# Kernel optimization log

Hardware: AMD Instinct MI355X
Metric: run time of the kernel (lower is better)

Reference implementation:

```python
import jax, jax.numpy as jnp
import numpy as np

N = 50000        # num_nodes
E = 200000       # num_edges
NODE_IN = 16
EDGE_IN = 8
H = 128          # hidden_dim (also per-head channels in GATConv)
HEADS = 4
L = 3            # num_layers
EPS = 1e-5
NEG_SLOPE = 0.2  # PyG GATConv default


def layer_norm(x, g, b):
    mu = jnp.mean(x, axis=-1, keepdims=True)
    v = jnp.var(x, axis=-1, keepdims=True)
    return (x - mu) * jax.lax.rsqrt(v + EPS) * g + b


def batch_norm_eval(x, g, b, rm, rv):
    return (x - rm) * jax.lax.rsqrt(rv + EPS) * g + b


def gat_layer(x, src, dst, W, a_src, a_dst, bias):
    # x: [N, H] -> per-head features [N, HEADS, H]
    xh = (x @ W).reshape(N, HEADS, H)
    al_src = jnp.sum(xh * a_src, axis=-1)  # [N, HEADS]
    al_dst = jnp.sum(xh * a_dst, axis=-1)  # [N, HEADS]
    alpha = jax.nn.leaky_relu(al_src[src] + al_dst[dst], NEG_SLOPE)  # [E', HEADS]
    # segment softmax over edges grouped by destination node
    m = jax.ops.segment_max(alpha, dst, num_segments=N)
    e = jnp.exp(alpha - m[dst])
    s = jax.ops.segment_sum(e, dst, num_segments=N)
    a = e / (s[dst] + 1e-16)
    msg = xh[src] * a[:, :, None]                 # [E', HEADS, H]
    out = jax.ops.segment_sum(msg, dst, num_segments=N)  # [N, HEADS, H]
    return jnp.mean(out, axis=1) + bias           # concat=False -> head mean


def setup_inputs() -> dict:
    key = jax.random.key(0)
    ks = jax.random.split(key, 24)
    s = 0.1
    inp = {
        "x": jax.random.normal(ks[0], (N, NODE_IN), jnp.float32),
        "edge_index": jax.random.randint(ks[1], (2, E), 0, N, jnp.int32),
        "edge_attr": jax.random.normal(ks[2], (E, EDGE_IN), jnp.float32),
        "shock_mask_nodes": jax.random.randint(ks[3], (N,), 0, 2, jnp.int32),
        # node encoder
        "enc_w": jax.random.normal(ks[4], (NODE_IN + 2, H), jnp.float32) * s,
        "enc_b": jnp.zeros((H,), jnp.float32),
        "enc_ln_g": jnp.ones((H,), jnp.float32),
        "enc_ln_b": jnp.zeros((H,), jnp.float32),
        # GAT layers (stacked over L)
        "gat_w": jax.random.normal(ks[5], (L, H, HEADS * H), jnp.float32) * s,
        "gat_att_src": jax.random.normal(ks[6], (L, HEADS, H), jnp.float32) * s,
        "gat_att_dst": jax.random.normal(ks[7], (L, HEADS, H), jnp.float32) * s,
        "gat_bias": jnp.zeros((L, H), jnp.float32),
        # BatchNorm (eval mode: running stats)
        "bn_g": jnp.ones((L, H), jnp.float32),
        "bn_b": jnp.zeros((L, H), jnp.float32),
        "bn_mean": jax.random.normal(ks[8], (L, H), jnp.float32) * 0.01,
        "bn_var": jnp.ones((L, H), jnp.float32),
        # edge MLP: (2H + EDGE_IN) -> H -> H//2 -> 1
        "em1_w": jax.random.normal(ks[9], (2 * H + EDGE_IN, H), jnp.float32) * s,
        "em1_b": jnp.zeros((H,), jnp.float32),
        "em_ln_g": jnp.ones((H,), jnp.float32),
        "em_ln_b": jnp.zeros((H,), jnp.float32),
        "em2_w": jax.random.normal(ks[10], (H, H // 2), jnp.float32) * s,
        "em2_b": jnp.zeros((H // 2,), jnp.float32),
        "em3_w": jax.random.normal(ks[11], (H // 2, 1), jnp.float32) * s,
        "em3_b": jnp.zeros((1,), jnp.float32),
    }
    return inp


def reference(x, edge_index, edge_attr, shock_mask_nodes,
              enc_w, enc_b, enc_ln_g, enc_ln_b,
              gat_w, gat_att_src, gat_att_dst, gat_bias,
              bn_g, bn_b, bn_mean, bn_var,
              em1_w, em1_b, em_ln_g, em_ln_b,
              em2_w, em2_b, em3_w, em3_b):
    src, dst = edge_index[0], edge_index[1]
    shock = shock_mask_nodes.astype(jnp.float32)[:, None]  # [N,1]
    # downstream indicator: scatter_add shock[src] into tgt, binarize
    down = jax.ops.segment_sum(shock[src, 0], dst, num_segments=N)
    down = (down > 0).astype(jnp.float32)[:, None]
    xa = jnp.concatenate([x, shock, down], axis=1)  # [N, NODE_IN+2]
    # node encoder (dropout off in eval)
    h = jax.nn.relu(layer_norm(xa @ enc_w + enc_b, enc_ln_g, enc_ln_b))
    # add self loops once (PyG GATConv default add_self_loops=True)
    loop = jnp.arange(N, dtype=src.dtype)
    src_sl = jnp.concatenate([src, loop])
    dst_sl = jnp.concatenate([dst, loop])
    for i in range(L):
        h = gat_layer(h, src_sl, dst_sl, gat_w[i], gat_att_src[i], gat_att_dst[i], gat_bias[i])
        h = batch_norm_eval(h, bn_g[i], bn_b[i], bn_mean[i], bn_var[i])
        if i < L - 1:
            h = jax.nn.relu(h)
    # edge predictor (note: source uses raw edge_attr, not augmented)
    edge_input = jnp.concatenate([h[src], h[dst], edge_attr], axis=1)  # [E, 2H+EDGE_IN]
    z = jax.nn.relu(layer_norm(edge_input @ em1_w + em1_b, em_ln_g, em_ln_b))
    z = jax.nn.relu(z @ em2_w + em2_b)
    delta = (z @ em3_w + em3_b)[:, 0]  # [E]
    return delta
```

## Files before the change

kernel.cpp:

```cpp
#include <hip/hip_runtime.h>
#include <hip/hip_bf16.h>


#define N_NODES 50000
#define N_EDGES 200000
#define ETOT    (N_EDGES + N_NODES)
#define HID     128
#define LN_EPS  1e-5f
#define NEG     0.2f
#define NSB     196

typedef __hip_bfloat16 bf16;
typedef __attribute__((ext_vector_type(8))) short v8s;
typedef __attribute__((ext_vector_type(4))) float v4f;
#define MFMA(a, b, c) __builtin_amdgcn_mfma_f32_16x16x32_bf16(a, b, c, 0, 0, 0)

__device__ __forceinline__ float b2f(unsigned short s) {
    return __uint_as_float(((unsigned int)s) << 16);
}
__device__ __forceinline__ unsigned short f2b(float f) {
    __hip_bfloat16 h = __float2bfloat16(f);
    return *reinterpret_cast<unsigned short*>(&h);
}
__device__ __forceinline__ unsigned int pack2(float a, float b) {
    return (unsigned int)f2b(a) | ((unsigned int)f2b(b) << 16);
}
__device__ __forceinline__ float pread(const void* p, size_t i, int isbf) {
    if (isbf) return b2f(((const unsigned short*)p)[i]);
    return ((const float*)p)[i];
}

__global__ void k_fill(float* out, int n, float v) {
    int i = blockIdx.x * blockDim.x + threadIdx.x;
    if (i < n) out[i] = v;
}

__global__ void k_detect(const unsigned short* __restrict__ xbuf,
                         int* __restrict__ flag) {
    int sane = 0;
    for (int j = threadIdx.x; j < 4096; j += 64) {
        unsigned short v = xbuf[2 * j];
        int e = (v >> 7) & 0xFF;
        if (v == 0 || (e > 96 && e < 160)) sane++;
    }
    for (int off = 32; off > 0; off >>= 1) sane += __shfl_down(sane, off);
    if (threadIdx.x == 0) flag[0] = (sane * 10 >= 4096 * 9) ? 1 : 0;
}

struct PrepArgs {
    const void *encw, *encb, *enlg, *enlb, *gatw, *asrc, *adst, *bias,
               *bng, *bnb, *bnm, *bnv, *em1w, *em1b, *emlg, *emlb,
               *em2w, *em2b, *em3w, *em3b;
};
#define PREP_ITEMS (150000 + 8193 + 1024 + 196608 + 32768 + 8192)
__global__ void k_prep(PrepArgs a, float* __restrict__ pool,
                       unsigned short* __restrict__ gwt,
                       unsigned short* __restrict__ uvt,
                       unsigned short* __restrict__ w2t,
                       float* __restrict__ down, int* __restrict__ deg,
                       int* __restrict__ fill, const int* __restrict__ flag) {
    int i = blockIdx.x * 256 + threadIdx.x;
    int bf = flag[0];
    if (i < 150000) {
        int which = i / 50000, idx = i - which * 50000;
        if (which == 0) down[idx] = 0.f;
        else if (which == 1) deg[idx] = 0;
        else fill[idx] = 0;
        return;
    }
    i -= 150000;
    if (i < 8193) {
        const void* s; int off;
        if      (i < 2304) { s = a.encw; off = 0;    }
        else if (i < 2432) { s = a.encb; off = 2304; }
        else if (i < 2560) { s = a.enlg; off = 2432; }
        else if (i < 2688) { s = a.enlb; off = 2560; }
        else if (i < 4224) { s = a.asrc; off = 2688; }
        else if (i < 5760) { s = a.adst; off = 4224; }
        else if (i < 6144) { s = a.bias; off = 5760; }
        else if (i < 6528) { s = a.bng;  off = 6144; }
        else if (i < 6912) { s = a.bnb;  off = 6528; }
        else if (i < 7296) { s = a.bnm;  off = 6912; }
        else if (i < 7680) { s = a.bnv;  off = 7296; }
        else if (i < 7808) { s = a.em1b; off = 7680; }
        else if (i < 7936) { s = a.emlg; off = 7808; }
        else if (i < 8064) { s = a.emlb; off = 7936; }
        else if (i < 8128) { s = a.em2b; off = 8064; }
        else if (i < 8192) { s = a.em3w; off = 8128; }
        else               { s = a.em3b; off = 8192; }
        pool[i] = pread(s, i - off, bf);
        return;
    }
    i -= 8193;
    if (i < 1024) {
        int k = i >> 7, c = i & 127;
        pool[8200 + i] = pread(a.em1w, (size_t)(256 + k) * 128 + c, bf);
        return;
    }
    i -= 1024;
    if (i < 196608) {
        int L = i >> 16, rem = i & 65535, n = rem >> 7, k = rem & 127;
        gwt[i] = f2b(pread(a.gatw, (size_t)L * 65536 + (size_t)k * 512 + n, bf));
        return;
    }
    i -= 196608;
    if (i < 32768) {
        int n = i >> 7, k = i & 127;
        float v = (n < 128) ? pread(a.em1w, (size_t)k * 128 + n, bf)
                            : pread(a.em1w, (size_t)(128 + k) * 128 + (n - 128), bf);
        uvt[i] = f2b(v);
        return;
    }
    i -= 32768;
    if (i < 8192) {
        int n = i >> 7, k = i & 127;
        w2t[i] = f2b(pread(a.em2w, (size_t)k * 64 + n, bf));
    }
}

__global__ void k_graph(const int* __restrict__ ei, const int* __restrict__ shock,
                        float* __restrict__ down, int* __restrict__ deg) {
    int e = blockIdx.x * blockDim.x + threadIdx.x;
    if (e < ETOT) {
        int d = (e < N_EDGES) ? ei[N_EDGES + e] : (e - N_EDGES);
        atomicAdd(&deg[d], 1);
        if (e < N_EDGES && shock[ei[e]] != 0) down[d] = 1.f;
    }
}

__global__ __launch_bounds__(256) void k_scan1(
        const int* __restrict__ deg, int* __restrict__ bsum) {
    __shared__ int red[4];
    int b = blockIdx.x, t = threadIdx.x, lane = t & 63, w = t >> 6;
    int idx = b * 256 + t;
    int v = (idx < N_NODES) ? deg[idx] : 0;
#pragma unroll
    for (int off = 1; off < 64; off <<= 1) v += __shfl_xor(v, off);
    if (lane == 0) red[w] = v;
    __syncthreads();
    if (t == 0) bsum[b] = red[0] + red[1] + red[2] + red[3];
}

__global__ __launch_bounds__(256) void k_scan2(
        const int* __restrict__ deg, const int* __restrict__ bsum,
        int* __restrict__ row_start) {
    __shared__ int red[4];
    __shared__ int wsum[4];
    int b = blockIdx.x, t = threadIdx.x, lane = t & 63, w = t >> 6;
    int pv = (t < b) ? bsum[t] : 0;
    int sm = pv;
#pragma unroll
    for (int off = 1; off < 64; off <<= 1) sm += __shfl_xor(sm, off);
    if (lane == 0) red[w] = sm;
    int idx = b * 256 + t;
    int v = (idx < N_NODES) ? deg[idx] : 0;
    int inc = v;
#pragma unroll
    for (int off = 1; off < 64; off <<= 1) {
        int u = __shfl_up(inc, off);
        if (lane >= off) inc += u;
    }
    if (lane == 63) wsum[w] = inc;
    __syncthreads();
    int boff = red[0] + red[1] + red[2] + red[3];
    int wo = 0;
#pragma unroll
    for (int i = 0; i < 4; i++) if (i < w) wo += wsum[i];
    if (idx < N_NODES) row_start[idx] = boff + wo + (inc - v);
    if (b == 0 && t == 0) row_start[N_NODES] = ETOT;
}

__global__ void k_csr(const int* __restrict__ ei, const int* __restrict__ row_start,
                      int* __restrict__ fill, int* __restrict__ csr_src) {
    int e = blockIdx.x * blockDim.x + threadIdx.x;
    if (e < ETOT) {
        int s, d;
        if (e < N_EDGES) { s = ei[e]; d = ei[N_EDGES + e]; }
        else             { s = e - N_EDGES; d = s; }
        int pos = row_start[d] + atomicAdd(&fill[d], 1);
        csr_src[pos] = s;
    }
}

__global__ __launch_bounds__(256) void k_encoder(
        const void* __restrict__ xraw, const int* __restrict__ flag,
        const int* __restrict__ shock, const float* __restrict__ down,
        const float* __restrict__ enc_w, const float* __restrict__ enc_b,
        const float* __restrict__ ln_g, const float* __restrict__ ln_b,
        unsigned short* __restrict__ h) {
    __shared__ float sw[2304];
    __shared__ float sp[384];
    int t = threadIdx.x;
    for (int i = t; i < 2304; i += 256) sw[i] = enc_w[i];
    if (t < 128)      sp[t] = enc_b[t];
    else if (t < 256) sp[t] = ln_g[t - 128];
    if (t < 128)      sp[256 + t] = ln_b[t];
    __syncthreads();

    int w = t >> 6, l = t & 63;
    int n = blockIdx.x * 4 + w;
    int bf = flag[0];
    int c0 = 2 * l, c1 = c0 + 1;

    float xv = (l < 16) ? pread(xraw, (size_t)n * 16 + l, bf) : 0.f;
    float xs = (float)shock[n];
    float xd = down[n];

    float a0 = sp[c0], a1 = sp[c1];
#pragma unroll
    for (int k = 0; k < 16; k++) {
        float xk = __shfl(xv, k);
        a0 = fmaf(xk, sw[k * HID + c0], a0);
        a1 = fmaf(xk, sw[k * HID + c1], a1);
    }
    a0 = fmaf(xs, sw[16 * HID + c0], a0); a1 = fmaf(xs, sw[16 * HID + c1], a1);
    a0 = fmaf(xd, sw[17 * HID + c0], a0); a1 = fmaf(xd, sw[17 * HID + c1], a1);

    float s = a0 + a1, q = a0 * a0 + a1 * a1;
#pragma unroll
    for (int off = 1; off < 64; off <<= 1) {
        s += __shfl_xor(s, off);
        q += __shfl_xor(q, off);
    }
    float mu = s * (1.f / 128.f);
    float var = q * (1.f / 128.f) - mu * mu;
    float rstd = rsqrtf(var + LN_EPS);
    float v0 = fmaxf((a0 - mu) * rstd * sp[128 + c0] + sp[256 + c0], 0.f);
    float v1 = fmaxf((a1 - mu) * rstd * sp[128 + c1] + sp[256 + c1], 0.f);
    *(unsigned int*)&h[(size_t)n * HID + c0] = pack2(v0, v1);
}

__global__ __launch_bounds__(256, 4) void k_gemm(
        const unsigned short* __restrict__ A, const unsigned short* __restrict__ Wt,
        const float* __restrict__ asrc, const float* __restrict__ adst,
        unsigned short* __restrict__ C,
        float* __restrict__ al_s, float* __restrict__ al_d) {
    __shared__ __align__(16) unsigned short As[64 * 136];
    __shared__ float alp[64][4][2];
    int t = threadIdx.x;
    int lane = t & 63, w = t >> 6, l15 = lane & 15, q = lane >> 4;
    int m0 = blockIdx.x * 64, n0 = blockIdx.y * 128, head = blockIdx.y;
    int c0 = n0 + w * 32 + 2 * l15, c1 = c0 + 1;

    v8s b[2][4];
#pragma unroll
    for (int nt = 0; nt < 2; nt++)
#pragma unroll
        for (int kt = 0; kt < 4; kt++)
            b[nt][kt] = *(const v8s*)&Wt[(size_t)(c0 + nt) * 128 + kt * 32 + q * 8];
#pragma unroll
    for (int it = 0; it < 4; it++) {
        int c = t + it * 256;
        int row = c >> 4, ch = c & 15;
        v8s val = {0, 0, 0, 0, 0, 0, 0, 0};
        if (m0 + row < N_NODES)
            val = *(const v8s*)&A[(size_t)(m0 + row) * 128 + ch * 8];
        *(v8s*)&As[row * 136 + ch * 8] = val;
    }
    __syncthreads();

    v4f acc[4][2] = {};
#pragma unroll
    for (int kt = 0; kt < 4; kt++)
#pragma unroll
        for (int mt = 0; mt < 4; mt++) {
            v8s a = *(const v8s*)&As[(mt * 16 + l15) * 136 + kt * 32 + q * 8];
            acc[mt][0] = MFMA(a, b[0][kt], acc[mt][0]);
            acc[mt][1] = MFMA(a, b[1][kt], acc[mt][1]);
        }
#pragma unroll
    for (int mt = 0; mt < 4; mt++)
#pragma unroll
        for (int r = 0; r < 4; r++) {
            int node = m0 + mt * 16 + q * 4 + r;
            if (node < N_NODES)
                *(unsigned int*)&C[(size_t)node * 512 + c0] =
                    pack2(acc[mt][0][r], acc[mt][1][r]);
        }

    float ps0 = asrc[c0], ps1 = asrc[c1];
    float pd0 = adst[c0], pd1 = adst[c1];
#pragma unroll
    for (int mt = 0; mt < 4; mt++)
#pragma unroll
        for (int r = 0; r < 4; r++) {
            float vs = acc[mt][0][r] * ps0 + acc[mt][1][r] * ps1;
            float vd = acc[mt][0][r] * pd0 + acc[mt][1][r] * pd1;
#pragma unroll
            for (int off = 1; off < 16; off <<= 1) {
                vs += __shfl_xor(vs, off);
                vd += __shfl_xor(vd, off);
            }
            if (l15 == 0) {
                alp[mt * 16 + q * 4 + r][w][0] = vs;
                alp[mt * 16 + q * 4 + r][w][1] = vd;
            }
        }
    __syncthreads();
    if (t < 64) {
        int node = m0 + t;
        if (node < N_NODES) {
            float ss = alp[t][0][0] + alp[t][1][0] + alp[t][2][0] + alp[t][3][0];
            float sd = alp[t][0][1] + alp[t][1][1] + alp[t][2][1] + alp[t][3][1];
            al_s[node * 4 + head] = ss;
            al_d[node * 4 + head] = sd;
        }
    }
}

__global__ __launch_bounds__(256) void k_aggregate(
        const unsigned short* __restrict__ xh, const float* __restrict__ al_src,
        const float* __restrict__ al_dst,
        const int* __restrict__ row_start, const int* __restrict__ csr_src,
        const float* __restrict__ bias,
        const float* __restrict__ bn_g, const float* __restrict__ bn_b,
        const float* __restrict__ bn_m, const float* __restrict__ bn_v,
        unsigned short* __restrict__ h, int relu_flag) {
    int w = threadIdx.x >> 6, l = threadIdx.x & 63;
    int n = blockIdx.x * 4 + w;
    int hh = l >> 4, c8 = l & 15;
    int r0 = row_start[n], r1 = row_start[n + 1];
    float ad = al_dst[n * 4 + hh];
    float sh = 0.f;
    float acc[8] = {};
    int last = r1 - 1;
    int i0 = csr_src[r0];
    int i1 = csr_src[(r0 + 1 < r1) ? r0 + 1 : last];
    float aC = al_src[i0 * 4 + hh];
    v8s rC = *(const v8s*)&xh[(size_t)i0 * 512 + l * 8];
    for (int j = r0; j < r1; j++) {
        int i2 = csr_src[(j + 2 < r1) ? j + 2 : last];
        float aN = al_src[i1 * 4 + hh];
        v8s rN = *(const v8s*)&xh[(size_t)i1 * 512 + l * 8];
        float a = aC + ad;
        a = (a >= 0.f) ? a : NEG * a;
        float we = __expf(a);
        sh += we;
#pragma unroll
        for (int i = 0; i < 8; i++)
            acc[i] = fmaf(we, b2f((unsigned short)rC[i]), acc[i]);
        aC = aN; rC = rN; i1 = i2;
    }
    float inv = 1.f / (sh + 1e-16f);
#pragma unroll
    for (int i = 0; i < 8; i++) {
        acc[i] *= inv;
        acc[i] += __shfl_xor(acc[i], 16);
        acc[i] += __shfl_xor(acc[i], 32);
    }
    if (hh == 0) {
        int cbase = c8 * 8;
        short o[8];
#pragma unroll
        for (int i = 0; i < 8; i++) {
            int c = cbase + i;
            float v = 0.25f * acc[i] + bias[c];
            v = (v - bn_m[c]) * rsqrtf(bn_v[c] + LN_EPS) * bn_g[c] + bn_b[c];
            if (relu_flag) v = fmaxf(v, 0.f);
            o[i] = (short)f2b(v);
        }
        *(v8s*)&h[(size_t)n * 128 + cbase] = *(const v8s*)o;
    }
}

__global__ __launch_bounds__(256, 4) void k_uvgemm(
        const unsigned short* __restrict__ A, const unsigned short* __restrict__ Wt,
        unsigned short* __restrict__ UV) {
    __shared__ __align__(16) unsigned short As[64 * 136];
    int t = threadIdx.x;
    int lane = t & 63, w = t >> 6, l15 = lane & 15, q = lane >> 4;
    int m0 = blockIdx.x * 64, n0 = blockIdx.y * 128;
    int c0 = n0 + w * 32 + 2 * l15;

    v8s b[2][4];
#pragma unroll
    for (int nt = 0; nt < 2; nt++)
#pragma unroll
        for (int kt = 0; kt < 4; kt++)
            b[nt][kt] = *(const v8s*)&Wt[(size_t)(c0 + nt) * 128 + kt * 32 + q * 8];
#pragma unroll
    for (int it = 0; it < 4; it++) {
        int c = t + it * 256;
        int row = c >> 4, ch = c & 15;
        v8s val = {0, 0, 0, 0, 0, 0, 0, 0};
        if (m0 + row < N_NODES)
            val = *(const v8s*)&A[(size_t)(m0 + row) * 128 + ch * 8];
        *(v8s*)&As[row * 136 + ch * 8] = val;
    }
    __syncthreads();

    v4f acc[4][2] = {};
#pragma unroll
    for (int kt = 0; kt < 4; kt++)
#pragma unroll
        for (int mt = 0; mt < 4; mt++) {
            v8s a = *(const v8s*)&As[(mt * 16 + l15) * 136 + kt * 32 + q * 8];
            acc[mt][0] = MFMA(a, b[0][kt], acc[mt][0]);
            acc[mt][1] = MFMA(a, b[1][kt], acc[mt][1]);
        }
#pragma unroll
    for (int mt = 0; mt < 4; mt++)
#pragma unroll
        for (int r = 0; r < 4; r++) {
            int node = m0 + mt * 16 + q * 4 + r;
            if (node < N_NODES)
                *(unsigned int*)&UV[(size_t)node * 256 + c0] =
                    pack2(acc[mt][0][r], acc[mt][1][r]);
        }
}

__global__ __launch_bounds__(256) void k_edgemlp3(
        const unsigned short* __restrict__ UV, const int* __restrict__ ei,
        const void* __restrict__ eraw, const int* __restrict__ flag,
        const float* __restrict__ w1e, const float* __restrict__ em1b,
        const float* __restrict__ lng, const float* __restrict__ lnb,
        const unsigned short* __restrict__ w2t, const float* __restrict__ em2b,
        const float* __restrict__ em3w, const float* __restrict__ em3b,
        float* __restrict__ out) {
    __shared__ __align__(16) unsigned short za[64 * 136];
    __shared__ __align__(16) float w1e_s[1024];
    __shared__ __align__(16) unsigned short ea_s[64 * 8];
    __shared__ int idx_s[128];
    __shared__ float part[4][64];

    int t = threadIdx.x;
    int lane = t & 63, w = t >> 6, l15 = lane & 15, q = lane >> 4;
    int e0 = blockIdx.x * 64;
    int bf = flag[0];
    int cb = l15 * 8;

    float bc[8], lg[8], lb[8];
#pragma unroll
    for (int j = 0; j < 8; j++) {
        bc[j] = em1b[cb + j];
        lg[j] = lng[cb + j];
        lb[j] = lnb[cb + j];
    }

    for (int i = t; i < 1024; i += 256) w1e_s[i] = w1e[i];
    if (t < 64) {
        idx_s[t * 2]     = ei[e0 + t];
        idx_s[t * 2 + 1] = ei[N_EDGES + e0 + t];
        if (bf) {
            *(v8s*)&ea_s[t * 8] =
                *(const v8s*)((const unsigned short*)eraw + (size_t)(e0 + t) * 8);
        } else {
            short tmp[8];
#pragma unroll
            for (int j = 0; j < 8; j++)
                tmp[j] = (short)f2b(((const float*)eraw)[(size_t)(e0 + t) * 8 + j]);
            *(v8s*)&ea_s[t * 8] = *(const v8s*)tmp;
        }
    }
    __syncthreads();

#pragma unroll 1
    for (int i = 0; i < 4; i++) {
        int el = w * 16 + i * 4 + q;
        int src = idx_s[el * 2], dst = idx_s[el * 2 + 1];
        v8s uu = *(const v8s*)&UV[(size_t)src * 256 + cb];
        v8s vv = *(const v8s*)&UV[(size_t)dst * 256 + 128 + cb];
        v8s ea8 = *(const v8s*)&ea_s[el * 8];
        float eaf[8];
#pragma unroll
        for (int k = 0; k < 8; k++) eaf[k] = b2f((unsigned short)ea8[k]);
        float e[8] = {};
#pragma unroll
        for (int k = 0; k < 8; k++) {
            float4 wa = *(const float4*)&w1e_s[k * 128 + cb];
            float4 wb = *(const float4*)&w1e_s[k * 128 + cb + 4];
            e[0] = fmaf(eaf[k], wa.x, e[0]);
            e[1] = fmaf(eaf[k], wa.y, e[1]);
            e[2] = fmaf(eaf[k], wa.z, e[2]);
            e[3] = fmaf(eaf[k], wa.w, e[3]);
            e[4] = fmaf(eaf[k], wb.x, e[4]);
            e[5] = fmaf(eaf[k], wb.y, e[5]);
            e[6] = fmaf(eaf[k], wb.z, e[6]);
            e[7] = fmaf(eaf[k], wb.w, e[7]);
        }
        float z[8];
        float s = 0.f, qq = 0.f;
#pragma unroll
        for (int j = 0; j < 8; j++) {
            float zz = b2f((unsigned short)uu[j]) + b2f((unsigned short)vv[j])
                     + e[j] + bc[j];
            z[j] = zz;
            s += zz;
            qq = fmaf(zz, zz, qq);
        }
#pragma unroll
        for (int off = 1; off < 16; off <<= 1) {
            s  += __shfl_xor(s, off);
            qq += __shfl_xor(qq, off);
        }
        float mu = s * (1.f / 128.f);
        float var = qq * (1.f / 128.f) - mu * mu;
        float rstd = rsqrtf(var + LN_EPS);
        short o[8];
#pragma unroll
        for (int j = 0; j < 8; j++)
            o[j] = (short)f2b(fmaxf((z[j] - mu) * rstd * lg[j] + lb[j], 0.f));
        *(v8s*)&za[el * 136 + cb] = *(const v8s*)o;
    }
    __syncthreads();

    v8s b2[4];
#pragma unroll
    for (int kt = 0; kt < 4; kt++)
        b2[kt] = *(const v8s*)&w2t[(size_t)(w * 16 + l15) * 128 + kt * 32 + q * 8];
    v4f acc2[4] = {};
#pragma unroll
    for (int kt = 0; kt < 4; kt++)
#pragma unroll
        for (int mt = 0; mt < 4; mt++) {
            v8s a = *(const v8s*)&za[(mt * 16 + l15) * 136 + kt * 32 + q * 8];
            acc2[mt] = MFMA(a, b2[kt], acc2[mt]);
        }

    {
        int col = w * 16 + l15;
        float b2c = em2b[col], w3c = em3w[col];
#pragma unroll
        for (int mt = 0; mt < 4; mt++)
#pragma unroll
            for (int r = 0; r < 4; r++) {
                float vv = fmaxf(acc2[mt][r] + b2c, 0.f) * w3c;
#pragma unroll
                for (int off = 1; off < 16; off <<= 1) vv += __shfl_xor(vv, off);
                if (l15 == 0) part[w][mt * 16 + q * 4 + r] = vv;
            }
    }
    __syncthreads();
    if (t < 64)
        out[e0 + t] = part[0][t] + part[1][t] + part[2][t] + part[3][t]
                    + em3b[0];
}

extern "C" __attribute__((visibility("default")))
void kernel_launch(void* const* d_in, const int* in_sizes, int n_in,
                   void* d_out, int out_size, void* d_ws, size_t ws_size,
                   hipStream_t stream) {
    float* out = (float*)d_out;

    static const int EXP_SIZES[24] = {
        800000, 400000, 1600000, 50000, 2304, 128, 128, 128,
        196608, 1536, 1536, 384, 384, 384, 384, 384,
        33792, 128, 128, 128, 8192, 64, 64, 1};
    bool ok = (n_in == 24) && (out_size == N_EDGES);
    if (ok) for (int i = 0; i < 24; i++) ok = ok && (in_sizes[i] == EXP_SIZES[i]);
    if (!ok) {
        k_fill<<<(out_size + 255) / 256, 256, 0, stream>>>(out, out_size, 4.0f);
        return;
    }
    if (ws_size < (size_t)68000000) {
        k_fill<<<(out_size + 255) / 256, 256, 0, stream>>>(out, out_size, 8.0f);
        return;
    }

    const int* ei    = (const int*)d_in[1];
    const int* shock = (const int*)d_in[3];

    char* ws = (char*)d_ws;
    unsigned short* h_bf  = (unsigned short*)(ws + 0);
    unsigned short* xh    = (unsigned short*)(ws + 12800000);
    unsigned short* UV    = xh;
    float* al_s    = (float*)(ws + 64000000);
    float* al_d    = (float*)(ws + 64800000);
    float* down    = (float*)(ws + 65600000);
    int*   deg     = (int*)  (ws + 65800000);
    int*   row_st  = (int*)  (ws + 66000000);
    int*   fill    = (int*)  (ws + 66200064);
    int*   csr_src = (int*)  (ws + 66400064);
    int*   flag    = (int*)  (ws + 67400064);
    unsigned short* gwt = (unsigned short*)(ws + 67400128);
    unsigned short* uvt = (unsigned short*)(ws + 67793344);
    unsigned short* w2t = (unsigned short*)(ws + 67858880);
    float* pool    = (float*)(ws + 67875264);
    int*   bsum    = (int*)  (ws + 67912160);

    float* cencw = pool + 0;    float* cencb = pool + 2304;
    float* cenlg = pool + 2432; float* cenlb = pool + 2560;
    float* casrc = pool + 2688; float* cadst = pool + 4224;
    float* cbias = pool + 5760; float* cbng  = pool + 6144;
    float* cbnb  = pool + 6528; float* cbnm  = pool + 6912;
    float* cbnv  = pool + 7296; float* cem1b = pool + 7680;
    float* cemlg = pool + 7808; float* cemlb = pool + 7936;
    float* cem2b = pool + 8064; float* cem3w = pool + 8128;
    float* cem3b = pool + 8192;
    float* w1e   = pool + 8200;

    k_detect<<<1, 64, 0, stream>>>((const unsigned short*)d_in[0], flag);

    PrepArgs pa;
    pa.encw = d_in[4];  pa.encb = d_in[5];  pa.enlg = d_in[6];  pa.enlb = d_in[7];
    pa.gatw = d_in[8];  pa.asrc = d_in[9];  pa.adst = d_in[10]; pa.bias = d_in[11];
    pa.bng  = d_in[12]; pa.bnb  = d_in[13]; pa.bnm  = d_in[14]; pa.bnv  = d_in[15];
    pa.em1w = d_in[16]; pa.em1b = d_in[17]; pa.emlg = d_in[18]; pa.emlb = d_in[19];
    pa.em2w = d_in[20]; pa.em2b = d_in[21]; pa.em3w = d_in[22]; pa.em3b = d_in[23];
    k_prep<<<(PREP_ITEMS + 255) / 256, 256, 0, stream>>>(
        pa, pool, gwt, uvt, w2t, down, deg, fill, flag);

    k_graph<<<(ETOT + 255) / 256, 256, 0, stream>>>(ei, shock, down, deg);
    k_scan1<<<NSB, 256, 0, stream>>>(deg, bsum);
    k_scan2<<<NSB, 256, 0, stream>>>(deg, bsum, row_st);
    k_csr<<<(ETOT + 255) / 256, 256, 0, stream>>>(ei, row_st, fill, csr_src);
    k_encoder<<<N_NODES / 4, 256, 0, stream>>>(
        d_in[0], flag, shock, down, cencw, cencb, cenlg, cenlb, h_bf);
    for (int i = 0; i < 3; i++) {
        k_gemm<<<dim3(782, 4), 256, 0, stream>>>(
            h_bf, gwt + (size_t)i * 65536, casrc + i * 512, cadst + i * 512,
            xh, al_s, al_d);
        k_aggregate<<<N_NODES / 4, 256, 0, stream>>>(
            xh, al_s, al_d, row_st, csr_src,
            cbias + i * 128, cbng + i * 128, cbnb + i * 128,
            cbnm + i * 128, cbnv + i * 128, h_bf, (i < 2) ? 1 : 0);
    }
    k_uvgemm<<<dim3(782, 2), 256, 0, stream>>>(h_bf, uvt, UV);
    k_edgemlp3<<<N_EDGES / 64, 256, 0, stream>>>(
        UV, ei, d_in[2], flag, w1e, cem1b, cemlg, cemlb,
        w2t, cem2b, cem3w, cem3b, out);
}
```

Before: 465.1 us.

## Aggregate raw node features before GAT projection and fold attention vectors into weights

Each GAT layer now runs in a different order. Attention logits come from h times precomputed W·a vectors. Per-head softmax-weighted sums of the 128-dim bf16 h rows are aggregated into a 512-wide buffer, and one fused GEMM against a reshaped W then applies head mean, bias and batchnorm. The point is to stop gathering 512-wide projected rows per edge and to stop materializing the N×512 projected tensor before aggregation. The cost is a K=512 GEMM after aggregation and a 512-wide aggregate write. A separate change software-pipelines the gather loads in the edge MLP loop.

```diff
diff --git a/kernel.cpp b/kernel.cpp
--- a/kernel.cpp
+++ b/kernel.cpp
@@ -52,11 +52,12 @@
                *bng, *bnb, *bnm, *bnv, *em1w, *em1b, *emlg, *emlb,
                *em2w, *em2b, *em3w, *em3b;
 };
-#define PREP_ITEMS (150000 + 8193 + 1024 + 196608 + 32768 + 8192)
+#define PREP_ITEMS (150000 + 8193 + 1024 + 196608 + 32768 + 8192 + 3072)
 __global__ void k_prep(PrepArgs a, float* __restrict__ pool,
                        unsigned short* __restrict__ gwt,
                        unsigned short* __restrict__ uvt,
                        unsigned short* __restrict__ w2t,
+                       float* __restrict__ wl,
                        float* __restrict__ down, int* __restrict__ deg,
                        int* __restrict__ fill, const int* __restrict__ flag) {
     int i = blockIdx.x * 256 + threadIdx.x;
@@ -99,8 +100,9 @@
     }
     i -= 1024;
     if (i < 196608) {
-        int L = i >> 16, rem = i & 65535, n = rem >> 7, k = rem & 127;
-        gwt[i] = f2b(pread(a.gatw, (size_t)L * 65536 + (size_t)k * 512 + n, bf));
+        int L = i >> 16, rem = i & 65535, c = rem >> 9, k = rem & 511;
+        gwt[i] = f2b(pread(a.gatw,
+            (size_t)L * 65536 + (size_t)(k & 127) * 512 + (k >> 7) * 128 + c, bf));
         return;
     }
     i -= 196608;
@@ -115,6 +117,19 @@
     if (i < 8192) {
         int n = i >> 7, k = i & 127;
         w2t[i] = f2b(pread(a.em2w, (size_t)k * 64 + n, bf));
+        return;
+    }
+    i -= 8192;
+    if (i < 3072) {
+        int L = i >> 10, rem = i & 1023, sd = rem >> 9, hh = (rem >> 7) & 3,
+            kk = rem & 127;
+        const void* av = sd ? a.adst : a.asrc;
+        float acc = 0.f;
+        for (int c = 0; c < 128; c++)
+            acc += pread(a.gatw,
+                       (size_t)L * 65536 + (size_t)kk * 512 + hh * 128 + c, bf)
+                 * pread(av, (size_t)L * 512 + hh * 128 + c, bf);
+        wl[i] = acc;
     }
 }
 
@@ -230,137 +245,140 @@
     *(unsigned int*)&h[(size_t)n * HID + c0] = pack2(v0, v1);
 }
 
-__global__ __launch_bounds__(256, 4) void k_gemm(
-        const unsigned short* __restrict__ A, const unsigned short* __restrict__ Wt,
-        const float* __restrict__ asrc, const float* __restrict__ adst,
-        unsigned short* __restrict__ C,
+__global__ __launch_bounds__(256) void k_logits(
+        const unsigned short* __restrict__ h, const float* __restrict__ wl,
         float* __restrict__ al_s, float* __restrict__ al_d) {
-    __shared__ __align__(16) unsigned short As[64 * 136];
-    __shared__ float alp[64][4][2];
+    __shared__ float wls[1024];
     int t = threadIdx.x;
+    for (int i = t; i < 1024; i += 256) wls[i] = wl[i];
+    __syncthreads();
     int lane = t & 63, w = t >> 6, l15 = lane & 15, q = lane >> 4;
-    int m0 = blockIdx.x * 64, n0 = blockIdx.y * 128, head = blockIdx.y;
-    int c0 = n0 + w * 32 + 2 * l15, c1 = c0 + 1;
-
-    v8s b[2][4];
-#pragma unroll
-    for (int nt = 0; nt < 2; nt++)
-#pragma unroll
-        for (int kt = 0; kt < 4; kt++)
-            b[nt][kt] = *(const v8s*)&Wt[(size_t)(c0 + nt) * 128 + kt * 32 + q * 8];
-#pragma unroll
-    for (int it = 0; it < 4; it++) {
-        int c = t + it * 256;
-        int row = c >> 4, ch = c & 15;
-        v8s val = {0, 0, 0, 0, 0, 0, 0, 0};
-        if (m0 + row < N_NODES)
-            val = *(const v8s*)&A[(size_t)(m0 + row) * 128 + ch * 8];
-        *(v8s*)&As[row * 136 + ch * 8] = val;
-    }
-    __syncthreads();
-
-    v4f acc[4][2] = {};
-#pragma unroll
-    for (int kt = 0; kt < 4; kt++)
-#pragma unroll
-        for (int mt = 0; mt < 4; mt++) {
-            v8s a = *(const v8s*)&As[(mt * 16 + l15) * 136 + kt * 32 + q * 8];
-            acc[mt][0] = MFMA(a, b[0][kt], acc[mt][0]);
-            acc[mt][1] = MFMA(a, b[1][kt], acc[mt][1]);
-        }
-#pragma unroll
-    for (int mt = 0; mt < 4; mt++)
-#pragma unroll
-        for (int r = 0; r < 4; r++) {
-            int node = m0 + mt * 16 + q * 4 + r;
-            if (node < N_NODES)
-                *(unsigned int*)&C[(size_t)node * 512 + c0] =
-                    pack2(acc[mt][0][r], acc[mt][1][r]);
-        }
-
-    float ps0 = asrc[c0], ps1 = asrc[c1];
-    float pd0 = adst[c0], pd1 = adst[c1];
-#pragma unroll
-    for (int mt = 0; mt < 4; mt++)
-#pragma unroll
-        for (int r = 0; r < 4; r++) {
-            float vs = acc[mt][0][r] * ps0 + acc[mt][1][r] * ps1;
-            float vd = acc[mt][0][r] * pd0 + acc[mt][1][r] * pd1;
-#pragma unroll
-            for (int off = 1; off < 16; off <<= 1) {
-                vs += __shfl_xor(vs, off);
-                vd += __shfl_xor(vd, off);
-            }
-            if (l15 == 0) {
-                alp[mt * 16 + q * 4 + r][w][0] = vs;
-                alp[mt * 16 + q * 4 + r][w][1] = vd;
-            }
-        }
-    __syncthreads();
-    if (t < 64) {
-        int node = m0 + t;
-        if (node < N_NODES) {
-            float ss = alp[t][0][0] + alp[t][1][0] + alp[t][2][0] + alp[t][3][0];
-            float sd = alp[t][0][1] + alp[t][1][1] + alp[t][2][1] + alp[t][3][1];
-            al_s[node * 4 + head] = ss;
-            al_d[node * 4 + head] = sd;
-        }
-    }
-}
-
-__global__ __launch_bounds__(256) void k_aggregate(
-        const unsigned short* __restrict__ xh, const float* __restrict__ al_src,
+    int n = blockIdx.x * 16 + w * 4 + q;
+    v8s hv = *(const v8s*)&h[(size_t)n * 128 + l15 * 8];
+    float hf[8];
+#pragma unroll
+    for (int m = 0; m < 8; m++) hf[m] = b2f((unsigned short)hv[m]);
+    float p[8] = {};
+#pragma unroll
+    for (int j = 0; j < 8; j++) {
+        float4 wa = *(const float4*)&wls[j * 128 + l15 * 8];
+        float4 wb = *(const float4*)&wls[j * 128 + l15 * 8 + 4];
+        p[j] = fmaf(hf[0], wa.x, p[j]); p[j] = fmaf(hf[1], wa.y, p[j]);
+        p[j] = fmaf(hf[2], wa.z, p[j]); p[j] = fmaf(hf[3], wa.w, p[j]);
+        p[j] = fmaf(hf[4], wb.x, p[j]); p[j] = fmaf(hf[5], wb.y, p[j]);
+        p[j] = fmaf(hf[6], wb.z, p[j]); p[j] = fmaf(hf[7], wb.w, p[j]);
+    }
+#pragma unroll
+    for (int off = 1; off < 16; off <<= 1)
+#pragma unroll
+        for (int j = 0; j < 8; j++) p[j] += __shfl_xor(p[j], off);
+    if (l15 == 0) {
+        float4 vs = {p[0], p[1], p[2], p[3]};
+        float4 vd = {p[4], p[5], p[6], p[7]};
+        *(float4*)&al_s[n * 4] = vs;
+        *(float4*)&al_d[n * 4] = vd;
+    }
+}
+
+__global__ __launch_bounds__(256) void k_agg2(
+        const unsigned short* __restrict__ h, const float* __restrict__ al_src,
         const float* __restrict__ al_dst,
         const int* __restrict__ row_start, const int* __restrict__ csr_src,
+        unsigned short* __restrict__ agg) {
+    int w = threadIdx.x >> 6, l = threadIdx.x & 63;
+    int n = blockIdx.x * 4 + w;
+    int r0 = row_start[n], r1 = row_start[n + 1];
+    float4 ad4 = *(const float4*)&al_dst[n * 4];
+    float s0 = 0.f, s1 = 0.f, s2 = 0.f, s3 = 0.f;
+    float acc[4][2] = {};
+    int last = r1 - 1;
+    int i0 = csr_src[r0];
+    int i1 = csr_src[(r0 + 1 < r1) ? r0 + 1 : last];
+    float4 aC = *(const float4*)&al_src[i0 * 4];
+    unsigned int hC = *(const unsigned int*)&h[(size_t)i0 * 128 + 2 * l];
+    for (int j = r0; j < r1; j++) {
+        int i2 = csr_src[(j + 2 < r1) ? j + 2 : last];
+        float4 aN = *(const float4*)&al_src[i1 * 4];
+        unsigned int hN = *(const unsigned int*)&h[(size_t)i1 * 128 + 2 * l];
+        float h0 = b2f((unsigned short)(hC & 0xFFFFu));
+        float h1 = b2f((unsigned short)(hC >> 16));
+        float t0 = aC.x + ad4.x; t0 = (t0 >= 0.f) ? t0 : NEG * t0;
+        float t1 = aC.y + ad4.y; t1 = (t1 >= 0.f) ? t1 : NEG * t1;
+        float t2 = aC.z + ad4.z; t2 = (t2 >= 0.f) ? t2 : NEG * t2;
+        float t3 = aC.w + ad4.w; t3 = (t3 >= 0.f) ? t3 : NEG * t3;
+        float e0 = __expf(t0), e1 = __expf(t1), e2 = __expf(t2), e3 = __expf(t3);
+        s0 += e0; s1 += e1; s2 += e2; s3 += e3;
+        acc[0][0] = fmaf(e0, h0, acc[0][0]); acc[0][1] = fmaf(e0, h1, acc[0][1]);
+        acc[1][0] = fmaf(e1, h0, acc[1][0]); acc[1][1] = fmaf(e1, h1, acc[1][1]);
+        acc[2][0] = fmaf(e2, h0, acc[2][0]); acc[2][1] = fmaf(e2, h1, acc[2][1]);
+        acc[3][0] = fmaf(e3, h0, acc[3][0]); acc[3][1] = fmaf(e3, h1, acc[3][1]);
+        aC = aN; hC = hN; i1 = i2;
+    }
+    float inv0 = 1.f / (s0 + 1e-16f), inv1 = 1.f / (s1 + 1e-16f);
+    float inv2 = 1.f / (s2 + 1e-16f), inv3 = 1.f / (s3 + 1e-16f);
+    size_t base = (size_t)n * 512 + 2 * l;
+    *(unsigned int*)&agg[base]       = pack2(acc[0][0] * inv0, acc[0][1] * inv0);
+    *(unsigned int*)&agg[base + 128] = pack2(acc[1][0] * inv1, acc[1][1] * inv1);
+    *(unsigned int*)&agg[base + 256] = pack2(acc[2][0] * inv2, acc[2][1] * inv2);
+    *(unsigned int*)&agg[base + 384] = pack2(acc[3][0] * inv3, acc[3][1] * inv3);
+}
+
+__global__ __launch_bounds__(256, 4) void k_gemm2(
+        const unsigned short* __restrict__ A,
+        const unsigned short* __restrict__ Wt,
         const float* __restrict__ bias,
         const float* __restrict__ bn_g, const float* __restrict__ bn_b,
         const float* __restrict__ bn_m, const float* __restrict__ bn_v,
-        unsigned short* __restrict__ h, int relu_flag) {
-    int w = threadIdx.x >> 6, l = threadIdx.x & 63;
-    int n = blockIdx.x * 4 + w;
-    int hh = l >> 4, c8 = l & 15;
-    int r0 = row_start[n], r1 = row_start[n + 1];
-    float ad = al_dst[n * 4 + hh];
-    float sh = 0.f;
-    float acc[8] = {};
-    int last = r1 - 1;
-    int i0 = csr_src[r0];
-    int i1 = csr_src[(r0 + 1 < r1) ? r0 + 1 : last];
-    float aC = al_src[i0 * 4 + hh];
-    v8s rC = *(const v8s*)&xh[(size_t)i0 * 512 + l * 8];
-    for (int j = r0; j < r1; j++) {
-        int i2 = csr_src[(j + 2 < r1) ? j + 2 : last];
-        float aN = al_src[i1 * 4 + hh];
-        v8s rN = *(const v8s*)&xh[(size_t)i1 * 512 + l * 8];
-        float a = aC + ad;
-        a = (a >= 0.f) ? a : NEG * a;
-        float we = __expf(a);
-        sh += we;
-#pragma unroll
-        for (int i = 0; i < 8; i++)
-            acc[i] = fmaf(we, b2f((unsigned short)rC[i]), acc[i]);
-        aC = aN; rC = rN; i1 = i2;
-    }
-    float inv = 1.f / (sh + 1e-16f);
-#pragma unroll
-    for (int i = 0; i < 8; i++) {
-        acc[i] *= inv;
-        acc[i] += __shfl_xor(acc[i], 16);
-        acc[i] += __shfl_xor(acc[i], 32);
-    }
-    if (hh == 0) {
-        int cbase = c8 * 8;
-        short o[8];
-#pragma unroll
-        for (int i = 0; i < 8; i++) {
-            int c = cbase + i;
-            float v = 0.25f * acc[i] + bias[c];
-            v = (v - bn_m[c]) * rsqrtf(bn_v[c] + LN_EPS) * bn_g[c] + bn_b[c];
-            if (relu_flag) v = fmaxf(v, 0.f);
-            o[i] = (short)f2b(v);
-        }
-        *(v8s*)&h[(size_t)n * 128 + cbase] = *(const v8s*)o;
-    }
+        unsigned short* __restrict__ hout, int relu_flag) {
+    __shared__ __align__(16) unsigned short As[64 * 136];
+    int t = threadIdx.x;
+    int lane = t & 63, w = t >> 6, l15 = lane & 15, q = lane >> 4;
+    int m0 = blockIdx.x * 64;
+    int c0 = w * 32 + 2 * l15, c1 = c0 + 1;
+
+    v4f acc[4][2] = {};
+#pragma unroll 1
+    for (int kc = 0; kc < 4; kc++) {
+        if (kc) __syncthreads();
+#pragma unroll
+        for (int it = 0; it < 4; it++) {
+            int c = t + it * 256;
+            int row = c >> 4, ch = c & 15;
+            v8s val = {0, 0, 0, 0, 0, 0, 0, 0};
+            if (m0 + row < N_NODES)
+                val = *(const v8s*)&A[(size_t)(m0 + row) * 512 + kc * 128 + ch * 8];
+            *(v8s*)&As[row * 136 + ch * 8] = val;
+        }
+        __syncthreads();
+#pragma unroll
+        for (int kt = 0; kt < 4; kt++) {
+            v8s b0 = *(const v8s*)&Wt[(size_t)c0 * 512 + kc * 128 + kt * 32 + q * 8];
+            v8s b1 = *(const v8s*)&Wt[(size_t)c1 * 512 + kc * 128 + kt * 32 + q * 8];
+#pragma unroll
+            for (int mt = 0; mt < 4; mt++) {
+                v8s a = *(const v8s*)&As[(mt * 16 + l15) * 136 + kt * 32 + q * 8];
+                acc[mt][0] = MFMA(a, b0, acc[mt][0]);
+                acc[mt][1] = MFMA(a, b1, acc[mt][1]);
+            }
+        }
+    }
+    float bi0 = bias[c0], bi1 = bias[c1];
+    float sc0 = rsqrtf(bn_v[c0] + LN_EPS) * bn_g[c0];
+    float sc1 = rsqrtf(bn_v[c1] + LN_EPS) * bn_g[c1];
+    float sh0 = bn_b[c0] - bn_m[c0] * sc0;
+    float sh1 = bn_b[c1] - bn_m[c1] * sc1;
+#pragma unroll
+    for (int mt = 0; mt < 4; mt++)
+#pragma unroll
+        for (int r = 0; r < 4; r++) {
+            int node = m0 + mt * 16 + q * 4 + r;
+            if (node < N_NODES) {
+                float v0 = (0.25f * acc[mt][0][r] + bi0) * sc0 + sh0;
+                float v1 = (0.25f * acc[mt][1][r] + bi1) * sc1 + sh1;
+                if (relu_flag) { v0 = fmaxf(v0, 0.f); v1 = fmaxf(v1, 0.f); }
+                *(unsigned int*)&hout[(size_t)node * 128 + c0] = pack2(v0, v1);
+            }
+        }
 }
 
 __global__ __launch_bounds__(256, 4) void k_uvgemm(
@@ -454,53 +472,64 @@
     }
     __syncthreads();
 
+    int elC = w * 16 + q;
+    {
+        int srcC = idx_s[elC * 2], dstC = idx_s[elC * 2 + 1];
+        v8s uuC = *(const v8s*)&UV[(size_t)srcC * 256 + cb];
+        v8s vvC = *(const v8s*)&UV[(size_t)dstC * 256 + 128 + cb];
+        v8s eaC = *(const v8s*)&ea_s[elC * 8];
 #pragma unroll 1
-    for (int i = 0; i < 4; i++) {
-        int el = w * 16 + i * 4 + q;
-        int src = idx_s[el * 2], dst = idx_s[el * 2 + 1];
-        v8s uu = *(const v8s*)&UV[(size_t)src * 256 + cb];
-        v8s vv = *(const v8s*)&UV[(size_t)dst * 256 + 128 + cb];
-        v8s ea8 = *(const v8s*)&ea_s[el * 8];
-        float eaf[8];
-#pragma unroll
-        for (int k = 0; k < 8; k++) eaf[k] = b2f((unsigned short)ea8[k]);
-        float e[8] = {};
-#pragma unroll
-        for (int k = 0; k < 8; k++) {
-            float4 wa = *(const float4*)&w1e_s[k * 128 + cb];
-            float4 wb = *(const float4*)&w1e_s[k * 128 + cb + 4];
-            e[0] = fmaf(eaf[k], wa.x, e[0]);
-            e[1] = fmaf(eaf[k], wa.y, e[1]);
-            e[2] = fmaf(eaf[k], wa.z, e[2]);
-            e[3] = fmaf(eaf[k], wa.w, e[3]);
-            e[4] = fmaf(eaf[k], wb.x, e[4]);
-            e[5] = fmaf(eaf[k], wb.y, e[5]);
-            e[6] = fmaf(eaf[k], wb.z, e[6]);
-            e[7] = fmaf(eaf[k], wb.w, e[7]);
-        }
-        float z[8];
-        float s = 0.f, qq = 0.f;
-#pragma unroll
-        for (int j = 0; j < 8; j++) {
-            float zz = b2f((unsigned short)uu[j]) + b2f((unsigned short)vv[j])
-                     + e[j] + bc[j];
-            z[j] = zz;
-            s += zz;
-            qq = fmaf(zz, zz, qq);
-        }
-#pragma unroll
-        for (int off = 1; off < 16; off <<= 1) {
-            s  += __shfl_xor(s, off);
-            qq += __shfl_xor(qq, off);
-        }
-        float mu = s * (1.f / 128.f);
-        float var = qq * (1.f / 128.f) - mu * mu;
-        float rstd = rsqrtf(var + LN_EPS);
-        short o[8];
-#pragma unroll
-        for (int j = 0; j < 8; j++)
-            o[j] = (short)f2b(fmaxf((z[j] - mu) * rstd * lg[j] + lb[j], 0.f));
-        *(v8s*)&za[el * 136 + cb] = *(const v8s*)o;
+        for (int i = 0; i < 4; i++) {
+            v8s uuN = uuC, vvN = vvC, eaN = eaC;
+            if (i < 3) {
+                int elN = elC + 4;
+                int srcN = idx_s[elN * 2], dstN = idx_s[elN * 2 + 1];
+                uuN = *(const v8s*)&UV[(size_t)srcN * 256 + cb];
+                vvN = *(const v8s*)&UV[(size_t)dstN * 256 + 128 + cb];
+                eaN = *(const v8s*)&ea_s[elN * 8];
+            }
+            float eaf[8];
+#pragma unroll
+            for (int k = 0; k < 8; k++) eaf[k] = b2f((unsigned short)eaC[k]);
+            float e[8] = {};
+#pragma unroll
+            for (int k = 0; k < 8; k++) {
+                float4 wa = *(const float4*)&w1e_s[k * 128 + cb];
+                float4 wb = *(const float4*)&w1e_s[k * 128 + cb + 4];
+                e[0] = fmaf(eaf[k], wa.x, e[0]);
+                e[1] = fmaf(eaf[k], wa.y, e[1]);
+                e[2] = fmaf(eaf[k], wa.z, e[2]);
+                e[3] = fmaf(eaf[k], wa.w, e[3]);
+                e[4] = fmaf(eaf[k], wb.x, e[4]);
+                e[5] = fmaf(eaf[k], wb.y, e[5]);
+                e[6] = fmaf(eaf[k], wb.z, e[6]);
+                e[7] = fmaf(eaf[k], wb.w, e[7]);
+            }
+            float z[8];
+            float s = 0.f, qq = 0.f;
+#pragma unroll
+            for (int j = 0; j < 8; j++) {
+                float zz = b2f((unsigned short)uuC[j]) + b2f((unsigned short)vvC[j])
+                         + e[j] + bc[j];
+                z[j] = zz;
+                s += zz;
+                qq = fmaf(zz, zz, qq);
+            }
+#pragma unroll
+            for (int off = 1; off < 16; off <<= 1) {
+                s  += __shfl_xor(s, off);
+                qq += __shfl_xor(qq, off);
+            }
+            float mu = s * (1.f / 128.f);
+            float var = qq * (1.f / 128.f) - mu * mu;
+            float rstd = rsqrtf(var + LN_EPS);
+            short o[8];
+#pragma unroll
+            for (int j = 0; j < 8; j++)
+                o[j] = (short)f2b(fmaxf((z[j] - mu) * rstd * lg[j] + lb[j], 0.f));
+            *(v8s*)&za[elC * 136 + cb] = *(const v8s*)o;
+            elC += 4; uuC = uuN; vvC = vvN; eaC = eaN;
+        }
     }
     __syncthreads();
 
@@ -562,8 +591,8 @@
 
     char* ws = (char*)d_ws;
     unsigned short* h_bf  = (unsigned short*)(ws + 0);
-    unsigned short* xh    = (unsigned short*)(ws + 12800000);
-    unsigned short* UV    = xh;
+    unsigned short* agg   = (unsigned short*)(ws + 12800000);
+    unsigned short* UV    = agg;
     float* al_s    = (float*)(ws + 64000000);
     float* al_d    = (float*)(ws + 64800000);
     float* down    = (float*)(ws + 65600000);
@@ -577,10 +606,10 @@
     unsigned short* w2t = (unsigned short*)(ws + 67858880);
     float* pool    = (float*)(ws + 67875264);
     int*   bsum    = (int*)  (ws + 67912160);
+    float* wl      = (float*)(ws + 67912960);
 
     float* cencw = pool + 0;    float* cencb = pool + 2304;
     float* cenlg = pool + 2432; float* cenlb = pool + 2560;
-    float* casrc = pool + 2688; float* cadst = pool + 4224;
     float* cbias = pool + 5760; float* cbng  = pool + 6144;
     float* cbnb  = pool + 6528; float* cbnm  = pool + 6912;
     float* cbnv  = pool + 7296; float* cem1b = pool + 7680;
@@ -598,7 +627,7 @@
     pa.em1w = d_in[16]; pa.em1b = d_in[17]; pa.emlg = d_in[18]; pa.emlb = d_in[19];
     pa.em2w = d_in[20]; pa.em2b = d_in[21]; pa.em3w = d_in[22]; pa.em3b = d_in[23];
     k_prep<<<(PREP_ITEMS + 255) / 256, 256, 0, stream>>>(
-        pa, pool, gwt, uvt, w2t, down, deg, fill, flag);
+        pa, pool, gwt, uvt, w2t, wl, down, deg, fill, flag);
 
     k_graph<<<(ETOT + 255) / 256, 256, 0, stream>>>(ei, shock, down, deg);
     k_scan1<<<NSB, 256, 0, stream>>>(deg, bsum);
@@ -607,11 +636,12 @@
     k_encoder<<<N_NODES / 4, 256, 0, stream>>>(
         d_in[0], flag, shock, down, cencw, cencb, cenlg, cenlb, h_bf);
     for (int i = 0; i < 3; i++) {
-        k_gemm<<<dim3(782, 4), 256, 0, stream>>>(
-            h_bf, gwt + (size_t)i * 65536, casrc + i * 512, cadst + i * 512,
-            xh, al_s, al_d);
-        k_aggregate<<<N_NODES / 4, 256, 0, stream>>>(
-            xh, al_s, al_d, row_st, csr_src,
+        k_logits<<<N_NODES / 16, 256, 0, stream>>>(
+            h_bf, wl + (size_t)i * 1024, al_s, al_d);
+        k_agg2<<<N_NODES / 4, 256, 0, stream>>>(
+            h_bf, al_s, al_d, row_st, csr_src, agg);
+        k_gemm2<<<782, 256, 0, stream>>>(
+            agg, gwt + (size_t)i * 65536,
             cbias + i * 128, cbng + i * 128, cbnb + i * 128,
             cbnm + i * 128, cbnv + i * 128, h_bf, (i < 2) ? 1 : 0);
     }
```

After: 502.7 us. +8.1%, slower.

## Process edge MLP in destination-sorted CSR order for gather locality

Applied to the files above, without the earlier changes.

The CSR array now stores edge ids instead of source ids, so aggregation resolves the source through an extra indirection into edge_index. The edge MLP walks edges in CSR (destination-sorted) order, which should improve cache reuse for the dst-side UV gathers, and scatters results back to the original edge positions. In exchange it launches more blocks to cover the self-loop slots, which do no useful work, adds a dependent load per edge in the aggregation loop, and turns the output writes and edge_attr reads into scattered accesses.

```diff
diff --git a/kernel.cpp b/kernel.cpp
--- a/kernel.cpp
+++ b/kernel.cpp
@@ -171,14 +171,12 @@
 }
 
 __global__ void k_csr(const int* __restrict__ ei, const int* __restrict__ row_start,
-                      int* __restrict__ fill, int* __restrict__ csr_src) {
+                      int* __restrict__ fill, int* __restrict__ csr) {
     int e = blockIdx.x * blockDim.x + threadIdx.x;
     if (e < ETOT) {
-        int s, d;
-        if (e < N_EDGES) { s = ei[e]; d = ei[N_EDGES + e]; }
-        else             { s = e - N_EDGES; d = s; }
+        int d = (e < N_EDGES) ? ei[N_EDGES + e] : (e - N_EDGES);
         int pos = row_start[d] + atomicAdd(&fill[d], 1);
-        csr_src[pos] = s;
+        csr[pos] = e;
     }
 }
 
@@ -311,7 +309,8 @@
 __global__ __launch_bounds__(256) void k_aggregate(
         const unsigned short* __restrict__ xh, const float* __restrict__ al_src,
         const float* __restrict__ al_dst,
-        const int* __restrict__ row_start, const int* __restrict__ csr_src,
+        const int* __restrict__ row_start, const int* __restrict__ csr,
+        const int* __restrict__ ei,
         const float* __restrict__ bias,
         const float* __restrict__ bn_g, const float* __restrict__ bn_b,
         const float* __restrict__ bn_m, const float* __restrict__ bn_v,
@@ -324,14 +323,17 @@
     float sh = 0.f;
     float acc[8] = {};
     int last = r1 - 1;
-    int i0 = csr_src[r0];
-    int i1 = csr_src[(r0 + 1 < r1) ? r0 + 1 : last];
-    float aC = al_src[i0 * 4 + hh];
-    v8s rC = *(const v8s*)&xh[(size_t)i0 * 512 + l * 8];
+    int eA = csr[r0];
+    int eB = csr[(r0 + 1 < r1) ? r0 + 1 : last];
+    int iA = (eA < N_EDGES) ? ei[eA] : eA - N_EDGES;
+    int iB = (eB < N_EDGES) ? ei[eB] : eB - N_EDGES;
+    float aC = al_src[iA * 4 + hh];
+    v8s rC = *(const v8s*)&xh[(size_t)iA * 512 + l * 8];
     for (int j = r0; j < r1; j++) {
-        int i2 = csr_src[(j + 2 < r1) ? j + 2 : last];
-        float aN = al_src[i1 * 4 + hh];
-        v8s rN = *(const v8s*)&xh[(size_t)i1 * 512 + l * 8];
+        int eN = csr[(j + 2 < r1) ? j + 2 : last];
+        float aN = al_src[iB * 4 + hh];
+        v8s rN = *(const v8s*)&xh[(size_t)iB * 512 + l * 8];
+        int iN = (eN < N_EDGES) ? ei[eN] : eN - N_EDGES;
         float a = aC + ad;
         a = (a >= 0.f) ? a : NEG * a;
         float we = __expf(a);
@@ -339,7 +341,7 @@
 #pragma unroll
         for (int i = 0; i < 8; i++)
             acc[i] = fmaf(we, b2f((unsigned short)rC[i]), acc[i]);
-        aC = aN; rC = rN; i1 = i2;
+        aC = aN; rC = rN; iB = iN;
     }
     float inv = 1.f / (sh + 1e-16f);
 #pragma unroll
@@ -411,6 +413,7 @@
 
 __global__ __launch_bounds__(256) void k_edgemlp3(
         const unsigned short* __restrict__ UV, const int* __restrict__ ei,
+        const int* __restrict__ csr,
         const void* __restrict__ eraw, const int* __restrict__ flag,
         const float* __restrict__ w1e, const float* __restrict__ em1b,
         const float* __restrict__ lng, const float* __restrict__ lnb,
@@ -421,11 +424,12 @@
     __shared__ __align__(16) float w1e_s[1024];
     __shared__ __align__(16) unsigned short ea_s[64 * 8];
     __shared__ int idx_s[128];
+    __shared__ int eid_s[64];
     __shared__ float part[4][64];
 
     int t = threadIdx.x;
     int lane = t & 63, w = t >> 6, l15 = lane & 15, q = lane >> 4;
-    int e0 = blockIdx.x * 64;
+    int p0 = blockIdx.x * 64;
     int bf = flag[0];
     int cb = l15 * 8;
 
@@ -439,17 +443,28 @@
 
     for (int i = t; i < 1024; i += 256) w1e_s[i] = w1e[i];
     if (t < 64) {
-        idx_s[t * 2]     = ei[e0 + t];
-        idx_s[t * 2 + 1] = ei[N_EDGES + e0 + t];
-        if (bf) {
-            *(v8s*)&ea_s[t * 8] =
-                *(const v8s*)((const unsigned short*)eraw + (size_t)(e0 + t) * 8);
+        int p = p0 + t;
+        int eid = (p < ETOT) ? csr[p] : N_EDGES;
+        int valid = (eid < N_EDGES);
+        int src = 0, dst = 0;
+        if (valid) { src = ei[eid]; dst = ei[N_EDGES + eid]; }
+        eid_s[t] = valid ? eid : -1;
+        idx_s[t * 2]     = src;
+        idx_s[t * 2 + 1] = dst;
+        if (valid) {
+            if (bf) {
+                *(v8s*)&ea_s[t * 8] =
+                    *(const v8s*)((const unsigned short*)eraw + (size_t)eid * 8);
+            } else {
+                short tmp[8];
+#pragma unroll
+                for (int j = 0; j < 8; j++)
+                    tmp[j] = (short)f2b(((const float*)eraw)[(size_t)eid * 8 + j]);
+                *(v8s*)&ea_s[t * 8] = *(const v8s*)tmp;
+            }
         } else {
-            short tmp[8];
-#pragma unroll
-            for (int j = 0; j < 8; j++)
-                tmp[j] = (short)f2b(((const float*)eraw)[(size_t)(e0 + t) * 8 + j]);
-            *(v8s*)&ea_s[t * 8] = *(const v8s*)tmp;
+            v8s zz = {0, 0, 0, 0, 0, 0, 0, 0};
+            *(v8s*)&ea_s[t * 8] = zz;
         }
     }
     __syncthreads();
@@ -531,9 +546,12 @@
             }
     }
     __syncthreads();
-    if (t < 64)
-        out[e0 + t] = part[0][t] + part[1][t] + part[2][t] + part[3][t]
-                    + em3b[0];
+    if (t < 64) {
+        int eid = eid_s[t];
+        if (eid >= 0)
+            out[eid] = part[0][t] + part[1][t] + part[2][t] + part[3][t]
+                     + em3b[0];
+    }
 }
 
 extern "C" __attribute__((visibility("default")))
@@ -570,7 +588,7 @@
     int*   deg     = (int*)  (ws + 65800000);
     int*   row_st  = (int*)  (ws + 66000000);
     int*   fill    = (int*)  (ws + 66200064);
-    int*   csr_src = (int*)  (ws + 66400064);
+    int*   csr     = (int*)  (ws + 66400064);
     int*   flag    = (int*)  (ws + 67400064);
     unsigned short* gwt = (unsigned short*)(ws + 67400128);
     unsigned short* uvt = (unsigned short*)(ws + 67793344);
@@ -603,7 +621,7 @@
     k_graph<<<(ETOT + 255) / 256, 256, 0, stream>>>(ei, shock, down, deg);
     k_scan1<<<NSB, 256, 0, stream>>>(deg, bsum);
     k_scan2<<<NSB, 256, 0, stream>>>(deg, bsum, row_st);
-    k_csr<<<(ETOT + 255) / 256, 256, 0, stream>>>(ei, row_st, fill, csr_src);
+    k_csr<<<(ETOT + 255) / 256, 256, 0, stream>>>(ei, row_st, fill, csr);
     k_encoder<<<N_NODES / 4, 256, 0, stream>>>(
         d_in[0], flag, shock, down, cencw, cencb, cenlg, cenlb, h_bf);
     for (int i = 0; i < 3; i++) {
@@ -611,12 +629,12 @@
             h_bf, gwt + (size_t)i * 65536, casrc + i * 512, cadst + i * 512,
             xh, al_s, al_d);
         k_aggregate<<<N_NODES / 4, 256, 0, stream>>>(
-            xh, al_s, al_d, row_st, csr_src,
+            xh, al_s, al_d, row_st, csr, ei,
             cbias + i * 128, cbng + i * 128, cbnb + i * 128,
             cbnm + i * 128, cbnv + i * 128, h_bf, (i < 2) ? 1 : 0);
     }
     k_uvgemm<<<dim3(782, 2), 256, 0, stream>>>(h_bf, uvt, UV);
-    k_edgemlp3<<<N_EDGES / 64, 256, 0, stream>>>(
-        UV, ei, d_in[2], flag, w1e, cem1b, cemlg, cemlb,
+    k_edgemlp3<<<(ETOT + 63) / 64, 256, 0, stream>>>(
+        UV, ei, csr, d_in[2], flag, w1e, cem1b, cemlg, cemlb,
         w2t, cem2b, cem3w, cem3b, out);
 }
```

Result: slower. 503.0 us (+8.2%).
